# Performance work log

Hardware: AMD Instinct MI355X
Metric: run time of the kernel (lower is better)

The kernel has to match this reference:

```python
import jax, jax.numpy as jnp
import numpy as np

EPS = 1e-8  # matches F.cosine_similarity eps


def setup_inputs() -> dict:
    key = jax.random.key(0)
    k1, k2 = jax.random.split(key)
    N, D = 4096, 256
    z1 = jax.random.normal(k1, (N, D), dtype=jnp.float32)
    z2 = jax.random.normal(k2, (N, D), dtype=jnp.float32)
    log_temperature = jnp.asarray(np.log(0.07), dtype=jnp.float32)
    return {"z1": z1, "z2": z2, "log_temperature": log_temperature}


def reference(z1, z2, log_temperature):
    N = z1.shape[0]
    z = jnp.concatenate([z1, z2], axis=0)                      # (2N, D)
    # cosine similarity: normalize once, then a single GEMM
    norm = jnp.maximum(jnp.linalg.norm(z, axis=-1, keepdims=True), EPS)
    zn = z / norm
    sim = zn @ zn.T                                            # (2N, 2N)
    diag = jnp.eye(2 * N, dtype=bool)
    sim = jnp.where(diag, -jnp.inf, sim)
    targets = jnp.concatenate([jnp.arange(N, 2 * N), jnp.arange(0, N)])
    logits = sim / jnp.exp(log_temperature)
    logp = jax.nn.log_softmax(logits, axis=-1)                 # (2N, 2N)
    loss = -jnp.mean(jnp.take_along_axis(logp, targets[:, None], axis=1))
    correct = jnp.sum(jnp.argmax(sim, axis=1) == targets).astype(jnp.float32) / 2.0
    return (loss, correct)
```

## Files before the change

kernel.cpp:

```cpp
#include <hip/hip_runtime.h>
#include <hip/hip_fp16.h>

#define NTOT 8192
#define NHALF 4096
#define DIM 256
#define LOG2E 1.4426950408889634f
#define NEG_BIG -1e30f
#define COLSPLIT 8
#define BM 128
#define BN 64
#define CPB (NTOT / COLSPLIT)

typedef _Float16 half8 __attribute__((ext_vector_type(8)));
typedef float floatx4 __attribute__((ext_vector_type(4)));

__global__ __launch_bounds__(256) void k_normalize(const float* __restrict__ z1,
                                                   const float* __restrict__ z2,
                                                   __half* __restrict__ zn) {
  int row = blockIdx.x * 4 + (threadIdx.x >> 6);
  int lane = threadIdx.x & 63;
  const float* src = (row < NHALF) ? (z1 + (size_t)row * DIM)
                                   : (z2 + (size_t)(row - NHALF) * DIM);
  float4 v = ((const float4*)src)[lane];
  float ss = v.x * v.x + v.y * v.y + v.z * v.z + v.w * v.w;
#pragma unroll
  for (int m = 1; m < 64; m <<= 1) ss += __shfl_xor(ss, m);
  float inv = 1.0f / fmaxf(sqrtf(ss), 1e-8f);
  __half2 h0, h1;
  h0.x = __float2half_rn(v.x * inv);
  h0.y = __float2half_rn(v.y * inv);
  h1.x = __float2half_rn(v.z * inv);
  h1.y = __float2half_rn(v.w * inv);
  __half2* dst = (__half2*)(zn + (size_t)row * DIM + lane * 4);
  dst[0] = h0;
  dst[1] = h1;
}

__global__ __launch_bounds__(256) void k_tsim(const __half* __restrict__ zn,
                                              float* __restrict__ tsim) {
  int row = blockIdx.x * 4 + (threadIdx.x >> 6);
  int lane = threadIdx.x & 63;
  int tgt = (row < NHALF) ? row + NHALF : row - NHALF;
  const __half2* a = (const __half2*)(zn + (size_t)row * DIM);
  const __half2* b = (const __half2*)(zn + (size_t)tgt * DIM);
  float s = 0.f;
#pragma unroll
  for (int j = 0; j < 2; j++) {
    float2 xf = __half22float2(a[lane * 2 + j]);
    float2 yf = __half22float2(b[lane * 2 + j]);
    s += xf.x * yf.x + xf.y * yf.y;
  }
#pragma unroll
  for (int m = 1; m < 64; m <<= 1) s += __shfl_xor(s, m);
  if (lane == 0) tsim[row] = s;
}

__global__ __launch_bounds__(256, 2) void k_main(const __half* __restrict__ zn,
                                                 const float* __restrict__ logT,
                                                 float* __restrict__ pM,
                                                 float* __restrict__ pL,
                                                 int* __restrict__ pI) {
  __shared__ uint4 lds[BN * 32];

  int bx = blockIdx.x;
  int rowTile = bx >> 3;
  int colq = bx & 7;
  int rowBase = rowTile * BM;
  int colBase = colq * CPB;
  int tid = threadIdx.x;
  int w = tid >> 6;
  int lane = tid & 63;
  int quad = lane >> 4;
  int cl = lane & 15;

  float invT = expf(-logT[0]);
  float kk = invT * LOG2E;

  half8 a[2][8];
  {
    int ar0 = rowBase + w * 32 + cl;
    int ar1 = ar0 + 16;
#pragma unroll
    for (int ks = 0; ks < 8; ks++) {
      a[0][ks] = *(const half8*)(zn + (size_t)ar0 * DIM + ks * 32 + quad * 8);
      a[1][ks] = *(const half8*)(zn + (size_t)ar1 * DIM + ks * 32 + quad * 8);
    }
  }

  float M[8], L[8];
  int AI[8];
#pragma unroll
  for (int s = 0; s < 8; s++) {
    M[s] = -3e38f;
    L[s] = 0.f;
    AI[s] = 0;
  }

  for (int t = 0; t < CPB / BN; t++) {
    __syncthreads();
#pragma unroll
    for (int i = 0; i < 8; i++) {
      int idx = tid + i * 256;
      int c = idx >> 5, ch = idx & 31;
      int g = colBase + t * BN + c;
      uint4 v = *(const uint4*)(zn + (size_t)g * DIM + ch * 8);
      lds[c * 32 + (ch ^ (c & 7))] = v;
    }
    __syncthreads();

    floatx4 acc[2][4];
#pragma unroll
    for (int rt = 0; rt < 2; rt++)
#pragma unroll
      for (int nt = 0; nt < 4; nt++) acc[rt][nt] = (floatx4){0.f, 0.f, 0.f, 0.f};

#pragma unroll
    for (int nt = 0; nt < 4; nt++) {
      int bc = nt * 16 + cl;
#pragma unroll
      for (int ks = 0; ks < 8; ks++) {
        int ch = ks * 4 + quad;
        half8 b = *(const half8*)&lds[bc * 32 + (ch ^ (bc & 7))];
        acc[0][nt] = __builtin_amdgcn_mfma_f32_16x16x32_f16(a[0][ks], b, acc[0][nt], 0, 0, 0);
        acc[1][nt] = __builtin_amdgcn_mfma_f32_16x16x32_f16(a[1][ks], b, acc[1][nt], 0, 0, 0);
      }
    }

    int colT = colBase + t * BN;
#pragma unroll
    for (int rt = 0; rt < 2; rt++) {
      int growB = rowBase + w * 32 + rt * 16 + quad * 4;
#pragma unroll
      for (int r = 0; r < 4; r++) {
        int grow = growB + r;
        float v0 = acc[rt][0][r], v1 = acc[rt][1][r];
        float v2 = acc[rt][2][r], v3 = acc[rt][3][r];
        int c0 = colT + cl;
        if (c0 == grow) v0 = NEG_BIG;
        if (c0 + 16 == grow) v1 = NEG_BIG;
        if (c0 + 32 == grow) v2 = NEG_BIG;
        if (c0 + 48 == grow) v3 = NEG_BIG;
        float mv = v0;
        int mi = c0;
        if (v1 > mv) { mv = v1; mi = c0 + 16; }
        if (v2 > mv) { mv = v2; mi = c0 + 32; }
        if (v3 > mv) { mv = v3; mi = c0 + 48; }
        int slot = rt * 4 + r;
        float Mo = M[slot];
        float Mn = fmaxf(Mo, mv);
        if (mv > Mo) AI[slot] = mi;
        float se = exp2f((v0 - Mn) * kk) + exp2f((v1 - Mn) * kk) +
                   exp2f((v2 - Mn) * kk) + exp2f((v3 - Mn) * kk);
        L[slot] = L[slot] * exp2f((Mo - Mn) * kk) + se;
        M[slot] = Mn;
      }
    }
  }

#pragma unroll
  for (int s = 0; s < 8; s++) {
    float m = M[s], l = L[s];
    int ai = AI[s];
#pragma unroll
    for (int sh = 1; sh < 16; sh <<= 1) {
      float om = __shfl_xor(m, sh);
      float ol = __shfl_xor(l, sh);
      int oi = __shfl_xor(ai, sh);
      float mn = fmaxf(m, om);
      l = l * exp2f((m - mn) * kk) + ol * exp2f((om - mn) * kk);
      if (om > m || (om == m && oi < ai)) ai = oi;
      m = mn;
    }
    M[s] = m;
    L[s] = l;
    AI[s] = ai;
  }

  if (cl == 0) {
#pragma unroll
    for (int rt = 0; rt < 2; rt++)
#pragma unroll
      for (int r = 0; r < 4; r++) {
        int grow = rowBase + w * 32 + rt * 16 + quad * 4 + r;
        int s = rt * 4 + r;
        int p = grow * COLSPLIT + colq;
        pM[p] = M[s];
        pL[p] = L[s];
        pI[p] = AI[s];
      }
  }
}

__global__ __launch_bounds__(256) void k_reduce(const float* __restrict__ pM,
                                                const float* __restrict__ pL,
                                                const int* __restrict__ pI,
                                                const float* __restrict__ tsim,
                                                const float* __restrict__ logT,
                                                float* __restrict__ out) {
  int row = blockIdx.x * 256 + threadIdx.x;
  float invT = expf(-logT[0]);
  float kk = invT * LOG2E;
  float m = -3e38f;
  int idx = 0;
#pragma unroll
  for (int q = 0; q < COLSPLIT; q++) {
    float mq = pM[row * COLSPLIT + q];
    if (mq > m) { m = mq; idx = pI[row * COLSPLIT + q]; }
  }
  float Lt = 0.f;
#pragma unroll
  for (int q = 0; q < COLSPLIT; q++)
    Lt += pL[row * COLSPLIT + q] * exp2f((pM[row * COLSPLIT + q] - m) * kk);
  int tgt = (row < NHALF) ? row + NHALF : row - NHALF;
  float logpt = (tsim[row] - m) * invT - logf(Lt);
  float loss = -logpt;
  float corr = (idx == tgt) ? 1.f : 0.f;

  __shared__ float sl[256], sc[256];
  sl[threadIdx.x] = loss;
  sc[threadIdx.x] = corr;
  __syncthreads();
  for (int s = 128; s > 0; s >>= 1) {
    if (threadIdx.x < s) {
      sl[threadIdx.x] += sl[threadIdx.x + s];
      sc[threadIdx.x] += sc[threadIdx.x + s];
    }
    __syncthreads();
  }
  if (threadIdx.x == 0) {
    atomicAdd(out + 0, sl[0] * (1.0f / (float)NTOT));
    atomicAdd(out + 1, sc[0] * 0.5f);
  }
}

extern "C" void kernel_launch(void* const* d_in, const int* in_sizes, int n_in,
                              void* d_out, int out_size, void* d_ws, size_t ws_size,
                              hipStream_t stream) {
  const float* z1 = (const float*)d_in[0];
  const float* z2 = (const float*)d_in[1];
  const float* logT = (const float*)d_in[2];
  float* out = (float*)d_out;

  char* ws = (char*)d_ws;
  __half* zn = (__half*)ws;
  float* tsim = (float*)(ws + 4 * 1024 * 1024);
  float* pM = (float*)(ws + 4 * 1024 * 1024 + 32 * 1024);
  float* pL = (float*)((char*)pM + NTOT * COLSPLIT * 4);
  int* pI = (int*)((char*)pL + NTOT * COLSPLIT * 4);

  k_normalize<<<NTOT / 4, 256, 0, stream>>>(z1, z2, zn);
  k_tsim<<<NTOT / 4, 256, 0, stream>>>(zn, tsim);
  k_main<<<(NTOT / BM) * COLSPLIT, 256, 0, stream>>>(zn, logT, pM, pL, pI);
  hipMemsetAsync(d_out, 0, 2 * sizeof(float), stream);
  k_reduce<<<NTOT / 256, 256, 0, stream>>>(pM, pL, pI, tsim, logT, out);
}
```

Baseline: 132.7 us.

## Use fixed softmax max, fuse prep kernels, direct-to-LDS loads, wider column split

Cosine similarities are bounded by 1, so the online softmax now drops the running max and sums exp((s-1)/T) directly. This removes the rescale exps and lets the cross-split merge become a plain sum. Normalization, the target-similarity dot product and output zeroing are fused into one prep kernel, which also replaces the memset. Tiles are loaded straight into LDS with global_load_lds, diagonal masking is applied only to tiles that contain the diagonal, the column split doubles to 16, and occupancy bounds go from 2 to 4. The fixed max risks underflow in the sum if the temperature were much smaller.

```diff
diff --git a/kernel.cpp b/kernel.cpp
--- a/kernel.cpp
+++ b/kernel.cpp
@@ -6,65 +6,110 @@
 #define DIM 256
 #define LOG2E 1.4426950408889634f
 #define NEG_BIG -1e30f
-#define COLSPLIT 8
+#define COLSPLIT 16
 #define BM 128
 #define BN 64
 #define CPB (NTOT / COLSPLIT)
+#define NTILES (CPB / BN)
 
 typedef _Float16 half8 __attribute__((ext_vector_type(8)));
 typedef float floatx4 __attribute__((ext_vector_type(4)));
 
-__global__ __launch_bounds__(256) void k_normalize(const float* __restrict__ z1,
-                                                   const float* __restrict__ z2,
-                                                   __half* __restrict__ zn) {
-  int row = blockIdx.x * 4 + (threadIdx.x >> 6);
-  int lane = threadIdx.x & 63;
-  const float* src = (row < NHALF) ? (z1 + (size_t)row * DIM)
-                                   : (z2 + (size_t)(row - NHALF) * DIM);
+__global__ __launch_bounds__(256) void k_prep(const float* __restrict__ z1,
+                                              const float* __restrict__ z2,
+                                              __half* __restrict__ zn,
+                                              float* __restrict__ tsim,
+                                              float* __restrict__ out) {
+  __shared__ float sh[4][256];
+  int w = threadIdx.x >> 6, lane = threadIdx.x & 63;
+  int p = blockIdx.x * 2 + (w >> 1);
+  int isZ2 = w & 1;
+  const float* src = (isZ2 ? z2 : z1) + (size_t)p * DIM;
   float4 v = ((const float4*)src)[lane];
   float ss = v.x * v.x + v.y * v.y + v.z * v.z + v.w * v.w;
 #pragma unroll
   for (int m = 1; m < 64; m <<= 1) ss += __shfl_xor(ss, m);
   float inv = 1.0f / fmaxf(sqrtf(ss), 1e-8f);
-  __half2 h0, h1;
-  h0.x = __float2half_rn(v.x * inv);
-  h0.y = __float2half_rn(v.y * inv);
-  h1.x = __float2half_rn(v.z * inv);
-  h1.y = __float2half_rn(v.w * inv);
+  __half h0 = __float2half_rn(v.x * inv), h1 = __float2half_rn(v.y * inv);
+  __half h2 = __float2half_rn(v.z * inv), h3 = __float2half_rn(v.w * inv);
+  int row = p + isZ2 * NHALF;
+  __half2 a2, b2;
+  a2.x = h0; a2.y = h1; b2.x = h2; b2.y = h3;
   __half2* dst = (__half2*)(zn + (size_t)row * DIM + lane * 4);
-  dst[0] = h0;
-  dst[1] = h1;
-}
-
-__global__ __launch_bounds__(256) void k_tsim(const __half* __restrict__ zn,
-                                              float* __restrict__ tsim) {
-  int row = blockIdx.x * 4 + (threadIdx.x >> 6);
-  int lane = threadIdx.x & 63;
-  int tgt = (row < NHALF) ? row + NHALF : row - NHALF;
-  const __half2* a = (const __half2*)(zn + (size_t)row * DIM);
-  const __half2* b = (const __half2*)(zn + (size_t)tgt * DIM);
-  float s = 0.f;
-#pragma unroll
-  for (int j = 0; j < 2; j++) {
-    float2 xf = __half22float2(a[lane * 2 + j]);
-    float2 yf = __half22float2(b[lane * 2 + j]);
-    s += xf.x * yf.x + xf.y * yf.y;
-  }
-#pragma unroll
-  for (int m = 1; m < 64; m <<= 1) s += __shfl_xor(s, m);
-  if (lane == 0) tsim[row] = s;
-}
-
-__global__ __launch_bounds__(256, 2) void k_main(const __half* __restrict__ zn,
+  dst[0] = a2;
+  dst[1] = b2;
+  float* s = sh[w];
+  s[lane * 4 + 0] = __half2float(h0);
+  s[lane * 4 + 1] = __half2float(h1);
+  s[lane * 4 + 2] = __half2float(h2);
+  s[lane * 4 + 3] = __half2float(h3);
+  __syncthreads();
+  if (w < 2) {
+    const float* sa = sh[w * 2];
+    const float* sb = sh[w * 2 + 1];
+    float4 xa = ((const float4*)sa)[lane];
+    float4 xb = ((const float4*)sb)[lane];
+    float d = xa.x * xb.x + xa.y * xb.y + xa.z * xb.z + xa.w * xb.w;
+#pragma unroll
+    for (int m = 1; m < 64; m <<= 1) d += __shfl_xor(d, m);
+    if (lane == 0) {
+      int pp = blockIdx.x * 2 + w;
+      tsim[pp] = d;
+      tsim[pp + NHALF] = d;
+    }
+  }
+  if (blockIdx.x == 0 && threadIdx.x < 2) out[threadIdx.x] = 0.0f;
+}
+
+template <bool DIAG>
+__device__ __forceinline__ void upd(const floatx4 (&acc)[2][4], int t, int colT, int cl,
+                                    int quad, int wRow0, float kk, float* L, float* BV,
+                                    int* BI) {
+#pragma unroll
+  for (int rt = 0; rt < 2; rt++) {
+    int growB = wRow0 + rt * 16 + quad * 4;
+#pragma unroll
+    for (int r = 0; r < 4; r++) {
+      int grow = growB + r;
+      float v0 = acc[rt][0][r], v1 = acc[rt][1][r];
+      float v2 = acc[rt][2][r], v3 = acc[rt][3][r];
+      if (DIAG) {
+        int c0 = colT + cl;
+        if (c0 == grow) v0 = NEG_BIG;
+        if (c0 + 16 == grow) v1 = NEG_BIG;
+        if (c0 + 32 == grow) v2 = NEG_BIG;
+        if (c0 + 48 == grow) v3 = NEG_BIG;
+      }
+      int slot = rt * 4 + r;
+      float e0 = __builtin_exp2f(__builtin_fmaf(v0, kk, -kk));
+      float e1 = __builtin_exp2f(__builtin_fmaf(v1, kk, -kk));
+      float e2 = __builtin_exp2f(__builtin_fmaf(v2, kk, -kk));
+      float e3 = __builtin_exp2f(__builtin_fmaf(v3, kk, -kk));
+      L[slot] += (e0 + e1) + (e2 + e3);
+      float m01 = fmaxf(v0, v1);
+      int i01 = (v1 > v0) ? 1 : 0;
+      float m23 = fmaxf(v2, v3);
+      int i23 = (v3 > v2) ? 3 : 2;
+      float mm = fmaxf(m01, m23);
+      int ii = (m23 > m01) ? i23 : i01;
+      if (mm > BV[slot]) {
+        BV[slot] = mm;
+        BI[slot] = t * 4 + ii;
+      }
+    }
+  }
+}
+
+__global__ __launch_bounds__(256, 4) void k_main(const __half* __restrict__ zn,
                                                  const float* __restrict__ logT,
-                                                 float* __restrict__ pM,
                                                  float* __restrict__ pL,
+                                                 float* __restrict__ pV,
                                                  int* __restrict__ pI) {
   __shared__ uint4 lds[BN * 32];
 
   int bx = blockIdx.x;
-  int rowTile = bx >> 3;
-  int colq = bx & 7;
+  int rowTile = bx >> 4;
+  int colq = bx & 15;
   int rowBase = rowTile * BM;
   int colBase = colq * CPB;
   int tid = threadIdx.x;
@@ -77,34 +122,37 @@
   float kk = invT * LOG2E;
 
   half8 a[2][8];
+  int wRow0 = rowBase + w * 32;
   {
-    int ar0 = rowBase + w * 32 + cl;
-    int ar1 = ar0 + 16;
+    int ar0 = wRow0 + cl;
 #pragma unroll
     for (int ks = 0; ks < 8; ks++) {
       a[0][ks] = *(const half8*)(zn + (size_t)ar0 * DIM + ks * 32 + quad * 8);
-      a[1][ks] = *(const half8*)(zn + (size_t)ar1 * DIM + ks * 32 + quad * 8);
-    }
-  }
-
-  float M[8], L[8];
-  int AI[8];
+      a[1][ks] = *(const half8*)(zn + (size_t)(ar0 + 16) * DIM + ks * 32 + quad * 8);
+    }
+  }
+
+  float L[8], BV[8];
+  int BI[8];
 #pragma unroll
   for (int s = 0; s < 8; s++) {
-    M[s] = -3e38f;
     L[s] = 0.f;
-    AI[s] = 0;
-  }
-
-  for (int t = 0; t < CPB / BN; t++) {
+    BV[s] = -3e38f;
+    BI[s] = 0;
+  }
+
+  for (int t = 0; t < NTILES; t++) {
+    int colT = colBase + t * BN;
     __syncthreads();
 #pragma unroll
     for (int i = 0; i < 8; i++) {
-      int idx = tid + i * 256;
-      int c = idx >> 5, ch = idx & 31;
-      int g = colBase + t * BN + c;
-      uint4 v = *(const uint4*)(zn + (size_t)g * DIM + ch * 8);
-      lds[c * 32 + (ch ^ (c & 7))] = v;
+      int cbase = w * 16 + i * 2;
+      int c = cbase + (lane >> 5);
+      int ch = (lane & 31) ^ (c & 7);
+      const void* gp = (const void*)(zn + (size_t)(colT + c) * DIM + ch * 8);
+      __builtin_amdgcn_global_load_lds(
+          (const __attribute__((address_space(1))) void*)gp,
+          (__attribute__((address_space(3))) void*)&lds[cbase * 32], 16, 0, 0);
     }
     __syncthreads();
 
@@ -126,95 +174,72 @@
       }
     }
 
-    int colT = colBase + t * BN;
-#pragma unroll
-    for (int rt = 0; rt < 2; rt++) {
-      int growB = rowBase + w * 32 + rt * 16 + quad * 4;
+    bool hasDiag = (colT <= wRow0 + 31) && (colT + BN - 1 >= wRow0);
+    if (hasDiag)
+      upd<true>(acc, t, colT, cl, quad, wRow0, kk, L, BV, BI);
+    else
+      upd<false>(acc, t, colT, cl, quad, wRow0, kk, L, BV, BI);
+  }
+
+#pragma unroll
+  for (int s = 0; s < 8; s++) {
+    float l = L[s];
+    float bv = BV[s];
+    int bi6 = BI[s];
+    int idx = ((bi6 >> 2) << 6) + ((bi6 & 3) << 4) + cl;
+#pragma unroll
+    for (int sh = 1; sh < 16; sh <<= 1) {
+      l += __shfl_xor(l, sh);
+      float ov = __shfl_xor(bv, sh);
+      int oi = __shfl_xor(idx, sh);
+      if (ov > bv || (ov == bv && oi < idx)) {
+        bv = ov;
+        idx = oi;
+      }
+    }
+    L[s] = l;
+    BV[s] = bv;
+    BI[s] = colBase + idx;
+  }
+
+  if (cl == 0) {
+#pragma unroll
+    for (int rt = 0; rt < 2; rt++)
 #pragma unroll
       for (int r = 0; r < 4; r++) {
-        int grow = growB + r;
-        float v0 = acc[rt][0][r], v1 = acc[rt][1][r];
-        float v2 = acc[rt][2][r], v3 = acc[rt][3][r];
-        int c0 = colT + cl;
-        if (c0 == grow) v0 = NEG_BIG;
-        if (c0 + 16 == grow) v1 = NEG_BIG;
-        if (c0 + 32 == grow) v2 = NEG_BIG;
-        if (c0 + 48 == grow) v3 = NEG_BIG;
-        float mv = v0;
-        int mi = c0;
-        if (v1 > mv) { mv = v1; mi = c0 + 16; }
-        if (v2 > mv) { mv = v2; mi = c0 + 32; }
-        if (v3 > mv) { mv = v3; mi = c0 + 48; }
-        int slot = rt * 4 + r;
-        float Mo = M[slot];
-        float Mn = fmaxf(Mo, mv);
-        if (mv > Mo) AI[slot] = mi;
-        float se = exp2f((v0 - Mn) * kk) + exp2f((v1 - Mn) * kk) +
-                   exp2f((v2 - Mn) * kk) + exp2f((v3 - Mn) * kk);
-        L[slot] = L[slot] * exp2f((Mo - Mn) * kk) + se;
-        M[slot] = Mn;
-      }
-    }
-  }
-
-#pragma unroll
-  for (int s = 0; s < 8; s++) {
-    float m = M[s], l = L[s];
-    int ai = AI[s];
-#pragma unroll
-    for (int sh = 1; sh < 16; sh <<= 1) {
-      float om = __shfl_xor(m, sh);
-      float ol = __shfl_xor(l, sh);
-      int oi = __shfl_xor(ai, sh);
-      float mn = fmaxf(m, om);
-      l = l * exp2f((m - mn) * kk) + ol * exp2f((om - mn) * kk);
-      if (om > m || (om == m && oi < ai)) ai = oi;
-      m = mn;
-    }
-    M[s] = m;
-    L[s] = l;
-    AI[s] = ai;
-  }
-
-  if (cl == 0) {
-#pragma unroll
-    for (int rt = 0; rt < 2; rt++)
-#pragma unroll
-      for (int r = 0; r < 4; r++) {
-        int grow = rowBase + w * 32 + rt * 16 + quad * 4 + r;
+        int grow = wRow0 + rt * 16 + quad * 4 + r;
         int s = rt * 4 + r;
         int p = grow * COLSPLIT + colq;
-        pM[p] = M[s];
         pL[p] = L[s];
-        pI[p] = AI[s];
-      }
-  }
-}
-
-__global__ __launch_bounds__(256) void k_reduce(const float* __restrict__ pM,
-                                                const float* __restrict__ pL,
+        pV[p] = BV[s];
+        pI[p] = BI[s];
+      }
+  }
+}
+
+__global__ __launch_bounds__(256) void k_reduce(const float* __restrict__ pL,
+                                                const float* __restrict__ pV,
                                                 const int* __restrict__ pI,
                                                 const float* __restrict__ tsim,
                                                 const float* __restrict__ logT,
                                                 float* __restrict__ out) {
   int row = blockIdx.x * 256 + threadIdx.x;
   float invT = expf(-logT[0]);
-  float kk = invT * LOG2E;
-  float m = -3e38f;
-  int idx = 0;
+  float Lt = 0.f;
+  float bv = -3e38f;
+  int bi = -1;
 #pragma unroll
   for (int q = 0; q < COLSPLIT; q++) {
-    float mq = pM[row * COLSPLIT + q];
-    if (mq > m) { m = mq; idx = pI[row * COLSPLIT + q]; }
-  }
-  float Lt = 0.f;
-#pragma unroll
-  for (int q = 0; q < COLSPLIT; q++)
-    Lt += pL[row * COLSPLIT + q] * exp2f((pM[row * COLSPLIT + q] - m) * kk);
+    Lt += pL[row * COLSPLIT + q];
+    float v = pV[row * COLSPLIT + q];
+    if (v > bv) {
+      bv = v;
+      bi = pI[row * COLSPLIT + q];
+    }
+  }
   int tgt = (row < NHALF) ? row + NHALF : row - NHALF;
-  float logpt = (tsim[row] - m) * invT - logf(Lt);
-  float loss = -logpt;
-  float corr = (idx == tgt) ? 1.f : 0.f;
+  float loss = invT + logf(Lt) - tsim[row] * invT;
+  float corr = (bi == tgt) ? 1.f : 0.f;
 
   __shared__ float sl[256], sc[256];
   sl[threadIdx.x] = loss;
@@ -244,13 +269,11 @@
   char* ws = (char*)d_ws;
   __half* zn = (__half*)ws;
   float* tsim = (float*)(ws + 4 * 1024 * 1024);
-  float* pM = (float*)(ws + 4 * 1024 * 1024 + 32 * 1024);
-  float* pL = (float*)((char*)pM + NTOT * COLSPLIT * 4);
-  int* pI = (int*)((char*)pL + NTOT * COLSPLIT * 4);
-
-  k_normalize<<<NTOT / 4, 256, 0, stream>>>(z1, z2, zn);
-  k_tsim<<<NTOT / 4, 256, 0, stream>>>(zn, tsim);
-  k_main<<<(NTOT / BM) * COLSPLIT, 256, 0, stream>>>(zn, logT, pM, pL, pI);
-  hipMemsetAsync(d_out, 0, 2 * sizeof(float), stream);
-  k_reduce<<<NTOT / 256, 256, 0, stream>>>(pM, pL, pI, tsim, logT, out);
-}
+  float* pL = (float*)(ws + 4 * 1024 * 1024 + 32 * 1024);
+  float* pV = (float*)((char*)pL + NTOT * COLSPLIT * 4);
+  int* pI = (int*)((char*)pV + NTOT * COLSPLIT * 4);
+
+  k_prep<<<NHALF / 2, 256, 0, stream>>>(z1, z2, zn, tsim, out);
+  k_main<<<(NTOT / BM) * COLSPLIT, 256, 0, stream>>>(zn, logT, pL, pV, pI);
+  k_reduce<<<NTOT / 256, 256, 0, stream>>>(pL, pV, pI, tsim, logT, out);
+}
```

New measurement: 503.0 us. 279% more time.
